# Optimization experiments

Hardware: AMD Instinct MI355X
Metric: run time of the kernel (lower is better)

The kernel has to match this reference:

```python
import jax, jax.numpy as jnp
import numpy as np

B, D, H = 131072, 8, 128  # batch, input_size (condition dims), hidden_size
DROPOUT_PROB = 0.1
NAN_FRAC = 0.15


def setup_inputs() -> dict:
    key = jax.random.key(0)
    k1, k2, k3, k4, k5, k6 = jax.random.split(key, 6)
    labels = jax.random.normal(k1, (B, D), dtype=jnp.float32)
    # NaN marks 'missing condition' -> falls back to embedding table row
    nan_mask = jax.random.uniform(k2, (B, D)) < NAN_FRAC
    labels = jnp.where(nan_mask, jnp.nan, labels)
    emb_w = jax.random.normal(k3, (D, H), dtype=jnp.float32) * 0.02  # embedding_drop.weight
    w1 = jax.random.normal(k4, (D, H), dtype=jnp.float32)           # Linear(1,H).weight per dim
    b1 = jax.random.normal(k5, (D, H), dtype=jnp.float32) * 0.02    # Linear(1,H).bias per dim
    w2 = jax.random.normal(k6, (D, H, H), dtype=jnp.float32) * 0.08 # Linear(H,H,bias=False).weight [out,in]
    return {"labels": labels, "emb_w": emb_w, "w1": w1, "b1": b1, "w2": w2,
            "train": 0, "unconditioned": 0}


def reference(labels, emb_w, w1, b1, w2, train, unconditioned):
    # drop mask per (sample, dim): NaN labels, optional random dropout, or everything
    if unconditioned:
        drop = jnp.ones(labels.shape, dtype=bool)
    else:
        drop = jnp.isnan(labels)
        if train:
            rkey = jax.random.fold_in(jax.random.key(0), 1)
            drop = drop | (jax.random.uniform(rkey, labels.shape) < DROPOUT_PROB)
    safe = jnp.where(drop, 0.0, labels)                      # [B,D] NaN-free
    # per-dim MLP, vectorized over dims: Linear(1,H) -> softmax(H) -> Linear(H,H)
    h1 = safe[:, :, None] * w1[None, :, :] + b1[None, :, :]  # [B,D,H]
    s = jax.nn.softmax(h1, axis=-1)                          # softmax over hidden (dim=1 of [N,H])
    mlp = jnp.einsum('bdh,dkh->bdk', s, w2)                  # [B,D,H]
    emb = jnp.where(drop[:, :, None], emb_w[None, :, :], mlp)
    if train:
        nkey = jax.random.fold_in(jax.random.key(0), 2)
        emb = emb + jax.random.normal(nkey, emb.shape, dtype=emb.dtype)
    return emb.sum(axis=1)                                   # [B,H]
```

## Files before the change

kernel.cpp:

```cpp
#include <hip/hip_runtime.h>
#include <hip/hip_bf16.h>

typedef __attribute__((ext_vector_type(4))) float f32x4;
typedef __attribute__((ext_vector_type(8))) short s16x8;

#define NB 131072
#define ND 8
#define NH 128
#define BLOCK_ROWS 128
#define W2S 136

__device__ __forceinline__ unsigned short f2bf(float f){
  unsigned u = __float_as_uint(f);
  u += 0x7fffu + ((u >> 16) & 1u);
  return (unsigned short)(u >> 16);
}

__global__ __launch_bounds__(256) void cvt_w2_kernel(const float4* __restrict__ src,
                                                     uint2* __restrict__ dst){
  int i = blockIdx.x * 256 + threadIdx.x;
  float4 v = src[i];
  uint2 o;
  o.x = (unsigned)f2bf(v.x) | ((unsigned)f2bf(v.y) << 16);
  o.y = (unsigned)f2bf(v.z) | ((unsigned)f2bf(v.w) << 16);
  dst[i] = o;
}

__global__ __launch_bounds__(256) void cond_embed_kernel(
    const float* __restrict__ labels,
    const float* __restrict__ emb_w,
    const float* __restrict__ w1,
    const float* __restrict__ b1,
    const unsigned short* __restrict__ w2b,
    const int* __restrict__ uncond_p,
    float* __restrict__ out)
{
  __shared__ __align__(16) unsigned short lds_w2[NH * W2S];
  __shared__ __align__(16) float lds_labels[BLOCK_ROWS * ND];
  __shared__ __align__(16) float lds_w1[ND * NH];
  __shared__ __align__(16) float lds_b1[ND * NH];
  __shared__ __align__(16) unsigned short lds_embT[NH * 8];

  const int tid  = threadIdx.x;
  const int wave = tid >> 6;
  const int lane = tid & 63;
  const int quad = lane >> 4;
  const int l16  = lane & 15;
  const int uncond = uncond_p[0];
  const int blockbase = blockIdx.x * BLOCK_ROWS;

  {
    const float4* src = (const float4*)(labels + blockbase * ND);
    ((float4*)lds_labels)[tid] = src[tid];
  }
  ((float4*)lds_w1)[tid] = ((const float4*)w1)[tid];
  ((float4*)lds_b1)[tid] = ((const float4*)b1)[tid];
  if (tid < NH){
    unsigned e0 = f2bf(emb_w[0*NH + tid]), e1 = f2bf(emb_w[1*NH + tid]);
    unsigned e2 = f2bf(emb_w[2*NH + tid]), e3 = f2bf(emb_w[3*NH + tid]);
    unsigned e4 = f2bf(emb_w[4*NH + tid]), e5 = f2bf(emb_w[5*NH + tid]);
    unsigned e6 = f2bf(emb_w[6*NH + tid]), e7 = f2bf(emb_w[7*NH + tid]);
    uint4 v;
    v.x = e0 | (e1 << 16);  v.y = e2 | (e3 << 16);
    v.z = e4 | (e5 << 16);  v.w = e6 | (e7 << 16);
    ((uint4*)lds_embT)[tid] = v;
  }

  f32x4 acc[2][8];
  #pragma unroll
  for (int mt = 0; mt < 2; ++mt)
    #pragma unroll
    for (int nt = 0; nt < 8; ++nt)
      acc[mt][nt] = (f32x4){0.f, 0.f, 0.f, 0.f};

  for (int d = 0; d < ND; ++d){
    __syncthreads();
    {
      const uint4* src = (const uint4*)(w2b + d * (NH * NH));
      #pragma unroll
      for (int c = tid; c < 2048; c += 256){
        int n = c >> 4, cc = c & 15;
        *((uint4*)&lds_w2[n * W2S + cc * 8]) = src[c];
      }
    }
    __syncthreads();

    s16x8 afrag[2][4];
    float zr[2][4];
    #pragma unroll
    for (int mt = 0; mt < 2; ++mt){
      int rib = wave * 32 + mt * 16 + l16;
      float x = lds_labels[rib * ND + d];
      bool drop = (uncond != 0) || (x != x);
      float xs = drop ? 0.f : x;
      float zp = 0.f;
      #pragma unroll
      for (int t = 0; t < 4; ++t){
        int kb = t * 32 + quad * 8;
        const float* w1p = &lds_w1[d * NH + kb];
        const float* b1p = &lds_b1[d * NH + kb];
        s16x8 a;
        #pragma unroll
        for (int j = 0; j < 8; ++j){
          float e = __expf(fmaf(xs, w1p[j], b1p[j]));
          zp += e;
          a[j] = (short)f2bf(e);
        }
        afrag[mt][t] = a;
      }
      zp += __shfl_xor(zp, 16);
      zp += __shfl_xor(zp, 32);
      float zinv = drop ? 0.f : (1.0f / zp);
      #pragma unroll
      for (int r = 0; r < 4; ++r) zr[mt][r] = __shfl(zinv, quad * 4 + r);
    }

    #pragma unroll
    for (int nt = 0; nt < 8; ++nt){
      const unsigned short* bb = &lds_w2[(nt * 16 + l16) * W2S + quad * 8];
      f32x4 t0 = (f32x4){0.f,0.f,0.f,0.f};
      f32x4 t1 = (f32x4){0.f,0.f,0.f,0.f};
      #pragma unroll
      for (int t = 0; t < 4; ++t){
        s16x8 b = *((const s16x8*)(bb + t * 32));
        t0 = __builtin_amdgcn_mfma_f32_16x16x32_bf16(afrag[0][t], b, t0, 0, 0, 0);
        t1 = __builtin_amdgcn_mfma_f32_16x16x32_bf16(afrag[1][t], b, t1, 0, 0, 0);
      }
      #pragma unroll
      for (int r = 0; r < 4; ++r){
        acc[0][nt][r] = fmaf(t0[r], zr[0][r], acc[0][nt][r]);
        acc[1][nt][r] = fmaf(t1[r], zr[1][r], acc[1][nt][r]);
      }
    }
  }

  s16x8 aex[2];
  #pragma unroll
  for (int mt = 0; mt < 2; ++mt){
    s16x8 a = (s16x8){0,0,0,0,0,0,0,0};
    if (quad == 0){
      int rib = wave * 32 + mt * 16 + l16;
      #pragma unroll
      for (int j = 0; j < 8; ++j){
        float x = lds_labels[rib * ND + j];
        bool drop = (uncond != 0) || (x != x);
        a[j] = drop ? (short)0x3F80 : (short)0;
      }
    }
    aex[mt] = a;
  }
  #pragma unroll
  for (int nt = 0; nt < 8; ++nt){
    s16x8 b = (s16x8){0,0,0,0,0,0,0,0};
    if (quad == 0) b = *((const s16x8*)&lds_embT[(nt * 16 + l16) * 8]);
    acc[0][nt] = __builtin_amdgcn_mfma_f32_16x16x32_bf16(aex[0], b, acc[0][nt], 0, 0, 0);
    acc[1][nt] = __builtin_amdgcn_mfma_f32_16x16x32_bf16(aex[1], b, acc[1][nt], 0, 0, 0);
  }

  #pragma unroll
  for (int mt = 0; mt < 2; ++mt){
    #pragma unroll
    for (int nt = 0; nt < 8; ++nt){
      #pragma unroll
      for (int r = 0; r < 4; ++r){
        int row = blockbase + wave * 32 + mt * 16 + quad * 4 + r;
        out[row * NH + nt * 16 + l16] = acc[mt][nt][r];
      }
    }
  }
}

extern "C" void kernel_launch(void* const* d_in, const int* in_sizes, int n_in,
                              void* d_out, int out_size, void* d_ws, size_t ws_size,
                              hipStream_t stream){
  const float* labels = (const float*)d_in[0];
  const float* emb_w  = (const float*)d_in[1];
  const float* w1     = (const float*)d_in[2];
  const float* b1     = (const float*)d_in[3];
  const float* w2     = (const float*)d_in[4];
  const int*   uncond = (const int*)d_in[6];
  (void)in_sizes; (void)n_in; (void)out_size; (void)ws_size;

  float* out = (float*)d_out;
  unsigned short* w2b = (unsigned short*)d_ws;

  cvt_w2_kernel<<<128, 256, 0, stream>>>((const float4*)w2, (uint2*)w2b);
  cond_embed_kernel<<<NB / BLOCK_ROWS, 256, 0, stream>>>(labels, emb_w, w1, b1, w2b, uncond, out);
}
```

Baseline: 149.8 us.

## Pre-swizzle W2, load via global_load_lds, compute softmax sums with MFMA

The conversion kernel now writes W2 in bf16 in a k-block-major layout, so each d-slice can be copied straight into LDS with global_load_lds and no padding. The softmax normaliser is computed with an MFMA against a ones vector instead of shuffles. Several other changes come with it: exp2 with prescaled w1/b1, a hardware reciprocal, a truncating perm-based bf16 pack, labels transposed in LDS, and an occupancy hint of 3 in launch_bounds. The truncating pack and the bf16 row sums add rounding error.

```diff
diff --git a/kernel.cpp b/kernel.cpp
--- a/kernel.cpp
+++ b/kernel.cpp
@@ -2,13 +2,27 @@
 #include <hip/hip_bf16.h>
 
 typedef __attribute__((ext_vector_type(4))) float f32x4;
+typedef __attribute__((ext_vector_type(4))) int   i32x4;
 typedef __attribute__((ext_vector_type(8))) short s16x8;
 
 #define NB 131072
 #define ND 8
 #define NH 128
-#define BLOCK_ROWS 128
-#define W2S 136
+#define BROWS 128
+
+#if __has_builtin(__builtin_amdgcn_exp2f)
+#define EXP2F(x) __builtin_amdgcn_exp2f(x)
+#define PRESCALE 1.4426950408889634f
+#else
+#define EXP2F(x) __expf(x)
+#define PRESCALE 1.0f
+#endif
+
+#if __has_builtin(__builtin_amdgcn_rcpf)
+#define RCPF(x) __builtin_amdgcn_rcpf(x)
+#else
+#define RCPF(x) (1.0f / (x))
+#endif
 
 __device__ __forceinline__ unsigned short f2bf(float f){
   unsigned u = __float_as_uint(f);
@@ -16,17 +30,26 @@
   return (unsigned short)(u >> 16);
 }
 
-__global__ __launch_bounds__(256) void cvt_w2_kernel(const float4* __restrict__ src,
-                                                     uint2* __restrict__ dst){
+__device__ __forceinline__ unsigned pk2(float lo, float hi){
+  return __builtin_amdgcn_perm(__float_as_uint(hi), __float_as_uint(lo), 0x07060302u);
+}
+
+__global__ __launch_bounds__(256) void cvt_w2_kernel(const float* __restrict__ src,
+                                                     uint4* __restrict__ dst){
   int i = blockIdx.x * 256 + threadIdx.x;
-  float4 v = src[i];
-  uint2 o;
-  o.x = (unsigned)f2bf(v.x) | ((unsigned)f2bf(v.y) << 16);
-  o.y = (unsigned)f2bf(v.z) | ((unsigned)f2bf(v.w) << 16);
+  int d = i >> 11, kb = (i >> 7) & 15, n = i & 127;
+  const float* s = src + ((d * 128 + n) * 128 + kb * 8);
+  float4 v0 = ((const float4*)s)[0];
+  float4 v1 = ((const float4*)s)[1];
+  uint4 o;
+  o.x = (unsigned)f2bf(v0.x) | ((unsigned)f2bf(v0.y) << 16);
+  o.y = (unsigned)f2bf(v0.z) | ((unsigned)f2bf(v0.w) << 16);
+  o.z = (unsigned)f2bf(v1.x) | ((unsigned)f2bf(v1.y) << 16);
+  o.w = (unsigned)f2bf(v1.z) | ((unsigned)f2bf(v1.w) << 16);
   dst[i] = o;
 }
 
-__global__ __launch_bounds__(256) void cond_embed_kernel(
+__global__ __launch_bounds__(256, 3) void cond_embed_kernel(
     const float* __restrict__ labels,
     const float* __restrict__ emb_w,
     const float* __restrict__ w1,
@@ -35,8 +58,8 @@
     const int* __restrict__ uncond_p,
     float* __restrict__ out)
 {
-  __shared__ __align__(16) unsigned short lds_w2[NH * W2S];
-  __shared__ __align__(16) float lds_labels[BLOCK_ROWS * ND];
+  __shared__ __align__(16) unsigned short lds_w2[NH * NH];
+  __shared__ __align__(16) float lds_lab[ND * BROWS];
   __shared__ __align__(16) float lds_w1[ND * NH];
   __shared__ __align__(16) float lds_b1[ND * NH];
   __shared__ __align__(16) unsigned short lds_embT[NH * 8];
@@ -47,14 +70,22 @@
   const int quad = lane >> 4;
   const int l16  = lane & 15;
   const int uncond = uncond_p[0];
-  const int blockbase = blockIdx.x * BLOCK_ROWS;
+  const int blockbase = blockIdx.x * BROWS;
 
   {
-    const float4* src = (const float4*)(labels + blockbase * ND);
-    ((float4*)lds_labels)[tid] = src[tid];
-  }
-  ((float4*)lds_w1)[tid] = ((const float4*)w1)[tid];
-  ((float4*)lds_b1)[tid] = ((const float4*)b1)[tid];
+    float4 v = ((const float4*)(labels + blockbase * ND))[tid];
+    int row = tid >> 1, dbase = (tid & 1) * 4;
+    lds_lab[(dbase + 0) * BROWS + row] = v.x;
+    lds_lab[(dbase + 1) * BROWS + row] = v.y;
+    lds_lab[(dbase + 2) * BROWS + row] = v.z;
+    lds_lab[(dbase + 3) * BROWS + row] = v.w;
+  }
+  {
+    float4 a = ((const float4*)w1)[tid];
+    float4 b = ((const float4*)b1)[tid];
+    ((float4*)lds_w1)[tid] = (float4){a.x * PRESCALE, a.y * PRESCALE, a.z * PRESCALE, a.w * PRESCALE};
+    ((float4*)lds_b1)[tid] = (float4){b.x * PRESCALE, b.y * PRESCALE, b.z * PRESCALE, b.w * PRESCALE};
+  }
   if (tid < NH){
     unsigned e0 = f2bf(emb_w[0*NH + tid]), e1 = f2bf(emb_w[1*NH + tid]);
     unsigned e2 = f2bf(emb_w[2*NH + tid]), e3 = f2bf(emb_w[3*NH + tid]);
@@ -73,56 +104,71 @@
     for (int nt = 0; nt < 8; ++nt)
       acc[mt][nt] = (f32x4){0.f, 0.f, 0.f, 0.f};
 
+  const s16x8 bones = (s16x8)((short)0x3F80);
+
   for (int d = 0; d < ND; ++d){
     __syncthreads();
     {
-      const uint4* src = (const uint4*)(w2b + d * (NH * NH));
-      #pragma unroll
-      for (int c = tid; c < 2048; c += 256){
-        int n = c >> 4, cc = c & 15;
-        *((uint4*)&lds_w2[n * W2S + cc * 8]) = src[c];
+      const unsigned short* g = w2b + d * (NH * NH);
+      #pragma unroll
+      for (int i = 0; i < 8; ++i){
+        int idx = tid + i * 256;
+        __builtin_amdgcn_global_load_lds(
+            (const __attribute__((address_space(1))) void*)(g + idx * 8),
+            (__attribute__((address_space(3))) void*)(lds_w2 + idx * 8),
+            16, 0, 0);
       }
     }
     __syncthreads();
 
     s16x8 afrag[2][4];
-    float zr[2][4];
+    f32x4 zr[2];
     #pragma unroll
     for (int mt = 0; mt < 2; ++mt){
       int rib = wave * 32 + mt * 16 + l16;
-      float x = lds_labels[rib * ND + d];
-      bool drop = (uncond != 0) || (x != x);
-      float xs = drop ? 0.f : x;
-      float zp = 0.f;
+      float x = lds_lab[d * BROWS + rib];
+      bool dropA = (uncond != 0) || (x != x);
+      float xs = dropA ? 0.f : x;
       #pragma unroll
       for (int t = 0; t < 4; ++t){
-        int kb = t * 32 + quad * 8;
-        const float* w1p = &lds_w1[d * NH + kb];
-        const float* b1p = &lds_b1[d * NH + kb];
-        s16x8 a;
-        #pragma unroll
-        for (int j = 0; j < 8; ++j){
-          float e = __expf(fmaf(xs, w1p[j], b1p[j]));
-          zp += e;
-          a[j] = (short)f2bf(e);
-        }
-        afrag[mt][t] = a;
-      }
-      zp += __shfl_xor(zp, 16);
-      zp += __shfl_xor(zp, 32);
-      float zinv = drop ? 0.f : (1.0f / zp);
-      #pragma unroll
-      for (int r = 0; r < 4; ++r) zr[mt][r] = __shfl(zinv, quad * 4 + r);
+        const float* w1p = &lds_w1[d * NH + t * 32 + quad * 8];
+        const float* b1p = &lds_b1[d * NH + t * 32 + quad * 8];
+        float e0 = EXP2F(fmaf(xs, w1p[0], b1p[0]));
+        float e1 = EXP2F(fmaf(xs, w1p[1], b1p[1]));
+        float e2 = EXP2F(fmaf(xs, w1p[2], b1p[2]));
+        float e3 = EXP2F(fmaf(xs, w1p[3], b1p[3]));
+        float e4 = EXP2F(fmaf(xs, w1p[4], b1p[4]));
+        float e5 = EXP2F(fmaf(xs, w1p[5], b1p[5]));
+        float e6 = EXP2F(fmaf(xs, w1p[6], b1p[6]));
+        float e7 = EXP2F(fmaf(xs, w1p[7], b1p[7]));
+        i32x4 ai;
+        ai[0] = (int)pk2(e0, e1);
+        ai[1] = (int)pk2(e2, e3);
+        ai[2] = (int)pk2(e4, e5);
+        ai[3] = (int)pk2(e6, e7);
+        afrag[mt][t] = __builtin_bit_cast(s16x8, ai);
+      }
+      f32x4 z = (f32x4){0.f, 0.f, 0.f, 0.f};
+      #pragma unroll
+      for (int t = 0; t < 4; ++t)
+        z = __builtin_amdgcn_mfma_f32_16x16x32_bf16(afrag[mt][t], bones, z, 0, 0, 0);
+      float4 xc = *(const float4*)&lds_lab[d * BROWS + wave * 32 + mt * 16 + quad * 4];
+      f32x4 zi;
+      zi[0] = ((uncond != 0) || (xc.x != xc.x)) ? 0.f : RCPF(z[0]);
+      zi[1] = ((uncond != 0) || (xc.y != xc.y)) ? 0.f : RCPF(z[1]);
+      zi[2] = ((uncond != 0) || (xc.z != xc.z)) ? 0.f : RCPF(z[2]);
+      zi[3] = ((uncond != 0) || (xc.w != xc.w)) ? 0.f : RCPF(z[3]);
+      zr[mt] = zi;
     }
 
     #pragma unroll
     for (int nt = 0; nt < 8; ++nt){
-      const unsigned short* bb = &lds_w2[(nt * 16 + l16) * W2S + quad * 8];
+      const unsigned short* bb = lds_w2 + (quad * NH + nt * 16 + l16) * 8;
       f32x4 t0 = (f32x4){0.f,0.f,0.f,0.f};
       f32x4 t1 = (f32x4){0.f,0.f,0.f,0.f};
       #pragma unroll
       for (int t = 0; t < 4; ++t){
-        s16x8 b = *((const s16x8*)(bb + t * 32));
+        s16x8 b = *((const s16x8*)(bb + t * 4 * NH * 8));
         t0 = __builtin_amdgcn_mfma_f32_16x16x32_bf16(afrag[0][t], b, t0, 0, 0, 0);
         t1 = __builtin_amdgcn_mfma_f32_16x16x32_bf16(afrag[1][t], b, t1, 0, 0, 0);
       }
@@ -137,12 +183,12 @@
   s16x8 aex[2];
   #pragma unroll
   for (int mt = 0; mt < 2; ++mt){
-    s16x8 a = (s16x8){0,0,0,0,0,0,0,0};
+    s16x8 a = (s16x8)((short)0);
     if (quad == 0){
       int rib = wave * 32 + mt * 16 + l16;
       #pragma unroll
       for (int j = 0; j < 8; ++j){
-        float x = lds_labels[rib * ND + j];
+        float x = lds_lab[j * BROWS + rib];
         bool drop = (uncond != 0) || (x != x);
         a[j] = drop ? (short)0x3F80 : (short)0;
       }
@@ -151,7 +197,7 @@
   }
   #pragma unroll
   for (int nt = 0; nt < 8; ++nt){
-    s16x8 b = (s16x8){0,0,0,0,0,0,0,0};
+    s16x8 b = (s16x8)((short)0);
     if (quad == 0) b = *((const s16x8*)&lds_embT[(nt * 16 + l16) * 8]);
     acc[0][nt] = __builtin_amdgcn_mfma_f32_16x16x32_bf16(aex[0], b, acc[0][nt], 0, 0, 0);
     acc[1][nt] = __builtin_amdgcn_mfma_f32_16x16x32_bf16(aex[1], b, acc[1][nt], 0, 0, 0);
@@ -184,6 +230,6 @@
   float* out = (float*)d_out;
   unsigned short* w2b = (unsigned short*)d_ws;
 
-  cvt_w2_kernel<<<128, 256, 0, stream>>>((const float4*)w2, (uint2*)w2b);
-  cond_embed_kernel<<<NB / BLOCK_ROWS, 256, 0, stream>>>(labels, emb_w, w1, b1, w2b, uncond, out);
-}
+  cvt_w2_kernel<<<64, 256, 0, stream>>>(w2, (uint4*)w2b);
+  cond_embed_kernel<<<NB / BROWS, 256, 0, stream>>>(labels, emb_w, w1, b1, w2b, uncond, out);
+}
```

New measurement: 132.6 us. 1.13x faster.
